# Kernel tuning notes

Measured on AMD Instinct MI355X. Metric: run time of the kernel, lower is better.

## Reference

```python
import jax, jax.numpy as jnp
import numpy as np

D_IN = 1024
D_OUT = 1024
NUM_HEADS = 16
HEAD_DIM = D_OUT // NUM_HEADS


def setup_inputs() -> dict:
    key = jax.random.key(0)
    k1, k2, k3, k4 = jax.random.split(key, 4)
    x = jax.random.normal(k1, (2, 2048, D_IN), dtype=jnp.float32)
    # Linear weights stored torch-style [out_features, in_features]
    W_qkv = jax.random.normal(k2, (3 * D_OUT, D_IN), dtype=jnp.float32) * (1.0 / np.sqrt(D_IN))
    W_out = jax.random.normal(k3, (D_OUT, D_OUT), dtype=jnp.float32) * (1.0 / np.sqrt(D_OUT))
    b_out = jax.random.normal(k4, (D_OUT,), dtype=jnp.float32) * 0.01
    return {"x": x, "W_qkv": W_qkv, "W_out": W_out, "b_out": b_out}


def reference(x, W_qkv, W_out, b_out):
    b, s, _ = x.shape
    qkv = jnp.einsum('bsi,oi->bso', x, W_qkv)  # [b, s, 3*d_out]
    q, k, v = jnp.split(qkv, 3, axis=-1)
    def to_heads(t):
        return t.reshape(b, s, NUM_HEADS, HEAD_DIM).transpose(0, 2, 1, 3)
    q, k, v = to_heads(q), to_heads(k), to_heads(v)
    # NOTE: original module does NOT scale by 1/sqrt(head_dim)
    scores = jnp.einsum('bhqd,bhkd->bhqk', q, k)
    causal = jnp.tril(jnp.ones((s, s), dtype=bool))  # True = keep
    scores = jnp.where(causal[None, None], scores, -jnp.inf)
    attn = jax.nn.softmax(scores, axis=-1)
    ctx = jnp.einsum('bhqk,bhkd->bhqd', attn, v)
    ctx = ctx.transpose(0, 2, 1, 3).reshape(b, s, D_OUT)
    return jnp.einsum('bso,po->bsp', ctx, W_out) + b_out
```

## Files before the change

kernel.cpp:

```cpp
#include <hip/hip_runtime.h>
#include <cstdint>
#include <cstddef>


typedef __attribute__((ext_vector_type(8))) short bf16x8;
typedef __attribute__((ext_vector_type(4))) float f32x4;

#define LOG2E 1.44269504f

#define MFMA16(a, b, c) __builtin_amdgcn_mfma_f32_16x16x32_bf16((a), (b), (c), 0, 0, 0)

#define GLDS16(g, s)                                                        \
  __builtin_amdgcn_global_load_lds(                                         \
      (const __attribute__((address_space(1))) void*)(g),                   \
      (__attribute__((address_space(3))) void*)(s), 16, 0, 0)

#if __has_builtin(__builtin_amdgcn_exp2f)
#define EXP2F(x) __builtin_amdgcn_exp2f(x)
#else
#define EXP2F(x) exp2f(x)
#endif

static __device__ __forceinline__ unsigned short f2bf(float f) {
  unsigned int u = __builtin_bit_cast(unsigned int, f);
  u += 0x7FFFu + ((u >> 16) & 1u);
  return (unsigned short)(u >> 16);
}

static __device__ __forceinline__ unsigned int pk2bf(float a, float b) {
  const unsigned int ua = __builtin_bit_cast(unsigned int, a) + 0x8000u;
  const unsigned int ub = __builtin_bit_cast(unsigned int, b) + 0x8000u;
  return __builtin_amdgcn_perm(ub, ua, 0x07060302);
}

__global__ __launch_bounds__(256) void cast_bf16(const float* __restrict__ x,
                                                 const float* __restrict__ wq,
                                                 const float* __restrict__ wo,
                                                 unsigned short* __restrict__ xb,
                                                 unsigned short* __restrict__ wqb,
                                                 unsigned short* __restrict__ wob)
{
  const int id = blockIdx.x * 256 + threadIdx.x;
  const float* src;
  unsigned short* dst;
  int off;
  if (id < 1048576)               { src = x;  dst = xb;  off = id; }
  else if (id < 1048576 + 786432) { src = wq; dst = wqb; off = id - 1048576; }
  else                            { src = wo; dst = wob; off = id - (1048576 + 786432); }
  float4 v = ((const float4*)src)[off];
  ushort4 o;
  o.x = f2bf(v.x); o.y = f2bf(v.y); o.z = f2bf(v.z); o.w = f2bf(v.w);
  ((ushort4*)dst)[off] = o;
}

template <int MODE>
__global__ __launch_bounds__(256) void gemm_bt(const unsigned short* __restrict__ A,
                                               const unsigned short* __restrict__ B,
                                               const float* __restrict__ bias,
                                               float* __restrict__ OutF,
                                               unsigned short* __restrict__ Qb,
                                               unsigned short* __restrict__ Kb,
                                               unsigned short* __restrict__ Vt)
{
  __shared__ unsigned short pool[8704];
  unsigned short* Asm = pool;
  unsigned short* Bsm = pool + 4096;

  const int tid  = threadIdx.x;
  const int wave = tid >> 6, lane = tid & 63, quad = lane >> 4, cl = lane & 15;
  const int wm = wave >> 1, wn = wave & 1;
  const int m0 = blockIdx.y * 128, n0 = blockIdx.x * 128;
  const int sr = lane >> 2, sc = lane & 3;

  f32x4 acc[4][4];
  #pragma unroll
  for (int i = 0; i < 4; ++i)
    #pragma unroll
    for (int j = 0; j < 4; ++j)
      #pragma unroll
      for (int r = 0; r < 4; ++r) acc[i][j][r] = 0.f;

  const int scs = (sc ^ ((sr >> 1) & 3)) * 8;
  const int rchunk = (quad ^ ((cl >> 1) & 3)) * 8;
  for (int k0 = 0; k0 < 1024; k0 += 32) {
    __syncthreads();
    #pragma unroll
    for (int ii = 0; ii < 2; ++ii) {
      const int r = wave * 32 + ii * 16 + sr;
      GLDS16(A + (size_t)(m0 + r) * 1024 + k0 + scs, &Asm[(wave * 32 + ii * 16) * 32]);
      GLDS16(B + (size_t)(n0 + r) * 1024 + k0 + scs, &Bsm[(wave * 32 + ii * 16) * 32]);
    }
    __syncthreads();

    bf16x8 af[4], bfr[4];
    #pragma unroll
    for (int mt = 0; mt < 4; ++mt)
      af[mt] = *(const bf16x8*)&Asm[(wm * 64 + mt * 16 + cl) * 32 + rchunk];
    #pragma unroll
    for (int nt = 0; nt < 4; ++nt)
      bfr[nt] = *(const bf16x8*)&Bsm[(wn * 64 + nt * 16 + cl) * 32 + rchunk];
    #pragma unroll
    for (int mt = 0; mt < 4; ++mt)
      #pragma unroll
      for (int nt = 0; nt < 4; ++nt)
        acc[mt][nt] = MFMA16(af[mt], bfr[nt], acc[mt][nt]);
  }

  if (MODE == 1) {
    const int part = n0 >> 10;
    const int bb = m0 >> 11, ss = m0 & 2047;
    if (part == 2) {
      #pragma unroll
      for (int half = 0; half < 2; ++half) {
        __syncthreads();
        if (wn == half) {
          #pragma unroll
          for (int mt = 0; mt < 4; ++mt)
            #pragma unroll
            for (int nt = 0; nt < 4; ++nt) {
              const int nl = nt * 16 + cl;
              const int ml = wm * 64 + mt * 16 + quad * 4;
              ushort4 pk;
              pk.x = f2bf(acc[mt][nt][0]); pk.y = f2bf(acc[mt][nt][1]);
              pk.z = f2bf(acc[mt][nt][2]); pk.w = f2bf(acc[mt][nt][3]);
              *(ushort4*)&pool[nl * 136 + ml] = pk;
            }
        }
        __syncthreads();
        const int row = tid >> 2, q4 = tid & 3;
        const int nglob = n0 + half * 64 + row;
        const int hh = (nglob >> 6) & 15, d = nglob & 63;
        unsigned short* drow = Vt + ((size_t)(bb * 16 + hh) * 64 + d) * 2048 + ss;
        #pragma unroll
        for (int i = 0; i < 4; ++i) {
          const bf16x8 v = *(const bf16x8*)&pool[row * 136 + q4 * 32 + i * 8];
          *(bf16x8*)(drow + q4 * 32 + i * 8) = v;
        }
      }
    } else {
      unsigned short* dst = (part == 0) ? Qb : Kb;
      const float sc2 = (part == 0) ? LOG2E : 1.0f;
      #pragma unroll
      for (int mt = 0; mt < 4; ++mt) {
        const int sbase = ss + wm * 64 + mt * 16 + quad * 4;
        #pragma unroll
        for (int nt = 0; nt < 4; ++nt) {
          const int n = n0 + wn * 64 + nt * 16 + cl;
          const int hh = (n >> 6) & 15, d = n & 63;
          #pragma unroll
          for (int r = 0; r < 4; ++r)
            dst[((size_t)(bb * 16 + hh) * 2048 + sbase + r) * 64 + d] =
                f2bf(acc[mt][nt][r] * sc2);
        }
      }
    }
  } else {
    #pragma unroll
    for (int mt = 0; mt < 4; ++mt) {
      const int mbase = m0 + wm * 64 + mt * 16 + quad * 4;
      #pragma unroll
      for (int nt = 0; nt < 4; ++nt) {
        const int n = n0 + wn * 64 + nt * 16 + cl;
        const float bv = bias[n];
        #pragma unroll
        for (int r = 0; r < 4; ++r)
          OutF[(size_t)(mbase + r) * 1024 + n] = acc[mt][nt][r] + bv;
      }
    }
  }
}

__global__ __launch_bounds__(256) void attn_mfma(const unsigned short* __restrict__ Qb,
                                                 const unsigned short* __restrict__ Kb,
                                                 const unsigned short* __restrict__ Vt,
                                                 unsigned short* __restrict__ CTX)
{
  __shared__ unsigned short Ksm[2][64 * 64];
  __shared__ unsigned short Vsm[2][64 * 64];
  __shared__ unsigned short Psm[4][32 * 40];

  const int tid  = threadIdx.x;
  const int wave = tid >> 6, lane = tid & 63, quad = lane >> 4, cl = lane & 15;

  const int L   = blockIdx.x;
  const int bh  = 4 * (L & 7) + ((L >> 3) & 3);
  const int b   = bh >> 4, h = bh & 15;
  const int i   = L >> 5;
  const int t   = (i < 8) ? (15 - i) : (i - 8);
  const int q0  = t * 128;
  const int qw0 = q0 + wave * 32;
  const size_t base = (size_t)bh * (2048 * 64);

  bf16x8 qf[2][2];
  #pragma unroll
  for (int mf = 0; mf < 2; ++mf)
    #pragma unroll
    for (int dk = 0; dk < 2; ++dk)
      qf[mf][dk] = *(const bf16x8*)(Qb + base + (size_t)(qw0 + mf * 16 + cl) * 64 +
                                    dk * 32 + quad * 8);

  f32x4 oacc[2][4];
  #pragma unroll
  for (int mf = 0; mf < 2; ++mf)
    #pragma unroll
    for (int dt = 0; dt < 4; ++dt)
      #pragma unroll
      for (int r = 0; r < 4; ++r) oacc[mf][dt][r] = 0.f;
  float lr[2][4] = {};

  bf16x8 ones;
  #pragma unroll
  for (int k = 0; k < 8; ++k) ones[k] = (short)0x3F80;

  const int lrow  = lane >> 3;
  const int lslot = (lane & 7) ^ lrow;
  const int nch = 2 * t + 2;

  #pragma unroll
  for (int ii = 0; ii < 2; ++ii) {
    const int r0 = wave * 16 + ii * 8;
    GLDS16(Kb + base + (size_t)(r0 + lrow) * 64 + lslot * 8, &Ksm[0][r0 * 64]);
    GLDS16(Vt + base + (size_t)(r0 + lrow) * 2048 + lslot * 8, &Vsm[0][r0 * 64]);
  }

  #pragma unroll 1
  for (int ch = 0; ch < nch; ++ch) {
    const int cur = ch & 1;
    __syncthreads();
    if (ch + 1 < nch) {
      const int j64n = (ch + 1) * 64;
      #pragma unroll
      for (int ii = 0; ii < 2; ++ii) {
        const int r0 = wave * 16 + ii * 8;
        GLDS16(Kb + base + (size_t)(j64n + r0 + lrow) * 64 + lslot * 8,
               &Ksm[cur ^ 1][r0 * 64]);
        GLDS16(Vt + base + (size_t)(r0 + lrow) * 2048 + j64n + lslot * 8,
               &Vsm[cur ^ 1][r0 * 64]);
      }
    }

    const int j64 = ch * 64;
    #pragma unroll
    for (int jli = 0; jli < 2; ++jli) {
      const int jl = jli * 32, jg0 = j64 + jl;
      if (jg0 > qw0 + 31) continue;

      bf16x8 kf[2][2];
      #pragma unroll
      for (int jf = 0; jf < 2; ++jf)
        #pragma unroll
        for (int dk = 0; dk < 2; ++dk) {
          const int jrow = jl + jf * 16 + cl;
          const int slot = (dk * 4 + quad) ^ (cl & 7);
          kf[jf][dk] = *(const bf16x8*)&Ksm[cur][jrow * 64 + slot * 8];
        }

      f32x4 st[2][2];
      #pragma unroll
      for (int jf = 0; jf < 2; ++jf)
        #pragma unroll
        for (int mf = 0; mf < 2; ++mf) {
          f32x4 z;
          #pragma unroll
          for (int r = 0; r < 4; ++r) z[r] = 0.f;
          z = MFMA16(kf[jf][0], qf[mf][0], z);
          st[jf][mf] = MFMA16(kf[jf][1], qf[mf][1], z);
        }

      const bool diag = (jg0 + 32 > qw0);
      #pragma unroll
      for (int jf = 0; jf < 2; ++jf)
        #pragma unroll
        for (int mf = 0; mf < 2; ++mf) {
          float p[4];
          if (diag) {
            const int qg = qw0 + mf * 16 + cl;
            #pragma unroll
            for (int r = 0; r < 4; ++r) {
              const int jg = jg0 + jf * 16 + quad * 4 + r;
              p[r] = (jg <= qg) ? EXP2F(st[jf][mf][r]) : 0.f;
            }
          } else {
            #pragma unroll
            for (int r = 0; r < 4; ++r) p[r] = EXP2F(st[jf][mf][r]);
          }
          uint2 w;
          w.x = pk2bf(p[0], p[1]);
          w.y = pk2bf(p[2], p[3]);
          *(uint2*)&Psm[wave][(mf * 16 + cl) * 40 + jf * 16 + quad * 4] = w;
        }

      bf16x8 vf[4];
      #pragma unroll
      for (int dt = 0; dt < 4; ++dt) {
        const int d = dt * 16 + cl;
        const int slot = ((jl >> 3) + quad) ^ (cl & 7);
        vf[dt] = *(const bf16x8*)&Vsm[cur][d * 64 + slot * 8];
      }

      bf16x8 pf[2];
      #pragma unroll
      for (int mf = 0; mf < 2; ++mf)
        pf[mf] = *(const bf16x8*)&Psm[wave][(mf * 16 + cl) * 40 + quad * 8];

      #pragma unroll
      for (int mf = 0; mf < 2; ++mf) {
        f32x4 z;
        #pragma unroll
        for (int r = 0; r < 4; ++r) z[r] = 0.f;
        const f32x4 ls = MFMA16(pf[mf], ones, z);
        #pragma unroll
        for (int r = 0; r < 4; ++r) lr[mf][r] += ls[r];
      }

      #pragma unroll
      for (int dt = 0; dt < 4; ++dt)
        #pragma unroll
        for (int mf = 0; mf < 2; ++mf)
          oacc[mf][dt] = MFMA16(pf[mf], vf[dt], oacc[mf][dt]);
    }
  }

  #pragma unroll
  for (int mf = 0; mf < 2; ++mf) {
    float inv[4];
    #pragma unroll
    for (int r = 0; r < 4; ++r) inv[r] = 1.f / lr[mf][r];
    #pragma unroll
    for (int dt = 0; dt < 4; ++dt)
      #pragma unroll
      for (int r = 0; r < 4; ++r)
        CTX[(size_t)(b * 2048 + qw0 + mf * 16 + quad * 4 + r) * 1024 +
            h * 64 + dt * 16 + cl] = f2bf(oacc[mf][dt][r] * inv[r]);
  }
}

extern "C" void kernel_launch(void* const* d_in, const int* in_sizes, int n_in,
                              void* d_out, int out_size, void* d_ws, size_t ws_size,
                              hipStream_t stream)
{
  const float* x    = (const float*)d_in[0];
  const float* Wqkv = (const float*)d_in[1];
  const float* Wout = (const float*)d_in[2];
  const float* bout = (const float*)d_in[3];
  float* out = (float*)d_out;

  char* ws = (char*)d_ws;
  unsigned short* xb  = (unsigned short*)(ws);
  unsigned short* wqb = (unsigned short*)(ws + 8388608);
  unsigned short* wob = (unsigned short*)(ws + 14680064);
  unsigned short* Qb  = (unsigned short*)(ws + 16777216);
  unsigned short* Kb  = (unsigned short*)(ws + 25165824);
  unsigned short* Vt  = (unsigned short*)(ws + 33554432);
  unsigned short* CTX = (unsigned short*)(ws + 41943040);

  cast_bf16<<<dim3(8192), dim3(256), 0, stream>>>(x, Wqkv, Wout, xb, wqb, wob);

  gemm_bt<1><<<dim3(24, 32), dim3(256), 0, stream>>>(xb, wqb, nullptr, nullptr, Qb, Kb, Vt);

  attn_mfma<<<dim3(512), dim3(256), 0, stream>>>(Qb, Kb, Vt, CTX);

  gemm_bt<0><<<dim3(8, 32), dim3(256), 0, stream>>>(CTX, wob, bout, out, nullptr, nullptr, nullptr);
}
```

Before: 204.0 us.

## Pair low/high query tiles per wave for causal balance; stage Q/K stores via LDS

The attention kernel now gives each wave two 16-row query tiles drawn from opposite ends of the sequence (g and 127-g), so every wave does a near-equal amount of causal work. Each block's chunk count becomes 32-p, and MFMA work for the low tile is skipped once its causal limit is passed. Separately, the QKV GEMM epilogue for Q and K now stages output through shared memory and writes 16-byte vectors instead of scattered 2-byte stores. The trade-offs are extra barriers and a larger LDS pool, plus some divergence-dependent branches inside the inner loop.

```diff
diff --git a/kernel.cpp b/kernel.cpp
--- a/kernel.cpp
+++ b/kernel.cpp
@@ -62,7 +62,7 @@
                                                unsigned short* __restrict__ Kb,
                                                unsigned short* __restrict__ Vt)
 {
-  __shared__ unsigned short pool[8704];
+  __shared__ unsigned short pool[9216];
   unsigned short* Asm = pool;
   unsigned short* Bsm = pool + 4096;
 
@@ -141,17 +141,27 @@
       unsigned short* dst = (part == 0) ? Qb : Kb;
       const float sc2 = (part == 0) ? LOG2E : 1.0f;
       #pragma unroll
-      for (int mt = 0; mt < 4; ++mt) {
-        const int sbase = ss + wm * 64 + mt * 16 + quad * 4;
-        #pragma unroll
-        for (int nt = 0; nt < 4; ++nt) {
-          const int n = n0 + wn * 64 + nt * 16 + cl;
-          const int hh = (n >> 6) & 15, d = n & 63;
+      for (int half = 0; half < 2; ++half) {
+        __syncthreads();
+        if (wn == half) {
           #pragma unroll
-          for (int r = 0; r < 4; ++r)
-            dst[((size_t)(bb * 16 + hh) * 2048 + sbase + r) * 64 + d] =
-                f2bf(acc[mt][nt][r] * sc2);
-        }
+          for (int mt = 0; mt < 4; ++mt)
+            #pragma unroll
+            for (int nt = 0; nt < 4; ++nt) {
+              const int nl = nt * 16 + cl;
+              const int ml = wm * 64 + mt * 16 + quad * 4;
+              #pragma unroll
+              for (int r = 0; r < 4; ++r)
+                pool[(ml + r) * 72 + nl] = f2bf(acc[mt][nt][r] * sc2);
+            }
+        }
+        __syncthreads();
+        const int m = tid >> 1, dh = (tid & 1) * 32;
+        const int hh = ((n0 + half * 64) >> 6) & 15;
+        unsigned short* drow = dst + ((size_t)(bb * 16 + hh) * 2048 + ss + m) * 64 + dh;
+        #pragma unroll
+        for (int i = 0; i < 4; ++i)
+          *(bf16x8*)(drow + i * 8) = *(const bf16x8*)&pool[m * 72 + dh + i * 8];
       }
     }
   } else {
@@ -182,22 +192,21 @@
   const int tid  = threadIdx.x;
   const int wave = tid >> 6, lane = tid & 63, quad = lane >> 4, cl = lane & 15;
 
-  const int L   = blockIdx.x;
-  const int bh  = 4 * (L & 7) + ((L >> 3) & 3);
-  const int b   = bh >> 4, h = bh & 15;
-  const int i   = L >> 5;
-  const int t   = (i < 8) ? (15 - i) : (i - 8);
-  const int q0  = t * 128;
-  const int qw0 = q0 + wave * 32;
+  const int L  = blockIdx.x;
+  const int bh = 4 * (L & 7) + ((L >> 3) & 3);
+  const int b  = bh >> 4, h = bh & 15;
+  const int p  = L >> 5;
+  const int g  = p * 4 + wave;
+  const int qlo = g * 16;
+  const int qhi = (127 - g) * 16;
   const size_t base = (size_t)bh * (2048 * 64);
 
   bf16x8 qf[2][2];
   #pragma unroll
-  for (int mf = 0; mf < 2; ++mf)
-    #pragma unroll
-    for (int dk = 0; dk < 2; ++dk)
-      qf[mf][dk] = *(const bf16x8*)(Qb + base + (size_t)(qw0 + mf * 16 + cl) * 64 +
-                                    dk * 32 + quad * 8);
+  for (int dk = 0; dk < 2; ++dk) {
+    qf[0][dk] = *(const bf16x8*)(Qb + base + (size_t)(qlo + cl) * 64 + dk * 32 + quad * 8);
+    qf[1][dk] = *(const bf16x8*)(Qb + base + (size_t)(qhi + cl) * 64 + dk * 32 + quad * 8);
+  }
 
   f32x4 oacc[2][4];
   #pragma unroll
@@ -214,7 +223,7 @@
 
   const int lrow  = lane >> 3;
   const int lslot = (lane & 7) ^ lrow;
-  const int nch = 2 * t + 2;
+  const int nch = 32 - p;
 
   #pragma unroll
   for (int ii = 0; ii < 2; ++ii) {
@@ -242,8 +251,10 @@
     const int j64 = ch * 64;
     #pragma unroll
     for (int jli = 0; jli < 2; ++jli) {
-      const int jl = jli * 32, jg0 = j64 + jl;
-      if (jg0 > qw0 + 31) continue;
+      const int jg0 = j64 + jli * 32;
+      if (jg0 > qhi + 15) continue;
+      const bool lowAct = (jg0 <= qlo + 15);
+      const int jl = jli * 32;
 
       bf16x8 kf[2][2];
       #pragma unroll
@@ -260,6 +271,7 @@
       for (int jf = 0; jf < 2; ++jf)
         #pragma unroll
         for (int mf = 0; mf < 2; ++mf) {
+          if (mf == 0 && !lowAct) continue;
           f32x4 z;
           #pragma unroll
           for (int r = 0; r < 4; ++r) z[r] = 0.f;
@@ -267,28 +279,31 @@
           st[jf][mf] = MFMA16(kf[jf][1], qf[mf][1], z);
         }
 
-      const bool diag = (jg0 + 32 > qw0);
-      #pragma unroll
-      for (int jf = 0; jf < 2; ++jf)
-        #pragma unroll
-        for (int mf = 0; mf < 2; ++mf) {
-          float p[4];
+      #pragma unroll
+      for (int mf = 0; mf < 2; ++mf) {
+        if (mf == 0 && !lowAct) continue;
+        const int qbase = mf ? qhi : qlo;
+        const bool diag = (jg0 + 32 > qbase);
+        #pragma unroll
+        for (int jf = 0; jf < 2; ++jf) {
+          float pv[4];
           if (diag) {
-            const int qg = qw0 + mf * 16 + cl;
+            const int qg = qbase + cl;
             #pragma unroll
             for (int r = 0; r < 4; ++r) {
               const int jg = jg0 + jf * 16 + quad * 4 + r;
-              p[r] = (jg <= qg) ? EXP2F(st[jf][mf][r]) : 0.f;
+              pv[r] = (jg <= qg) ? EXP2F(st[jf][mf][r]) : 0.f;
             }
           } else {
             #pragma unroll
-            for (int r = 0; r < 4; ++r) p[r] = EXP2F(st[jf][mf][r]);
+            for (int r = 0; r < 4; ++r) pv[r] = EXP2F(st[jf][mf][r]);
           }
           uint2 w;
-          w.x = pk2bf(p[0], p[1]);
-          w.y = pk2bf(p[2], p[3]);
+          w.x = pk2bf(pv[0], pv[1]);
+          w.y = pk2bf(pv[2], pv[3]);
           *(uint2*)&Psm[wave][(mf * 16 + cl) * 40 + jf * 16 + quad * 4] = w;
         }
+      }
 
       bf16x8 vf[4];
       #pragma unroll
@@ -298,31 +313,26 @@
         vf[dt] = *(const bf16x8*)&Vsm[cur][d * 64 + slot * 8];
       }
 
-      bf16x8 pf[2];
-      #pragma unroll
-      for (int mf = 0; mf < 2; ++mf)
-        pf[mf] = *(const bf16x8*)&Psm[wave][(mf * 16 + cl) * 40 + quad * 8];
-
       #pragma unroll
       for (int mf = 0; mf < 2; ++mf) {
+        if (mf == 0 && !lowAct) continue;
+        const bf16x8 pf = *(const bf16x8*)&Psm[wave][(mf * 16 + cl) * 40 + quad * 8];
         f32x4 z;
         #pragma unroll
         for (int r = 0; r < 4; ++r) z[r] = 0.f;
-        const f32x4 ls = MFMA16(pf[mf], ones, z);
+        const f32x4 ls = MFMA16(pf, ones, z);
         #pragma unroll
         for (int r = 0; r < 4; ++r) lr[mf][r] += ls[r];
-      }
-
-      #pragma unroll
-      for (int dt = 0; dt < 4; ++dt)
-        #pragma unroll
-        for (int mf = 0; mf < 2; ++mf)
-          oacc[mf][dt] = MFMA16(pf[mf], vf[dt], oacc[mf][dt]);
+        #pragma unroll
+        for (int dt = 0; dt < 4; ++dt)
+          oacc[mf][dt] = MFMA16(pf, vf[dt], oacc[mf][dt]);
+      }
     }
   }
 
   #pragma unroll
   for (int mf = 0; mf < 2; ++mf) {
+    const int qbase = mf ? qhi : qlo;
     float inv[4];
     #pragma unroll
     for (int r = 0; r < 4; ++r) inv[r] = 1.f / lr[mf][r];
@@ -330,7 +340,7 @@
     for (int dt = 0; dt < 4; ++dt)
       #pragma unroll
       for (int r = 0; r < 4; ++r)
-        CTX[(size_t)(b * 2048 + qw0 + mf * 16 + quad * 4 + r) * 1024 +
+        CTX[(size_t)(b * 2048 + qbase + quad * 4 + r) * 1024 +
             h * 64 + dt * 16 + cl] = f2bf(oacc[mf][dt][r] * inv[r]);
   }
 }
```

Result: slower. 209.4 us (+2.7%).
